# Kernel tuning notes

Hardware: AMD Instinct MI355X
Metric: run time of the kernel (lower is better)

The kernel has to match this reference:

```python
import jax, jax.numpy as jnp
import numpy as np

TEMP = 1.0
EULER_GAMMA = 0.5772156649015329
BIG = 1.0e9


def setup_inputs() -> dict:
    key = jax.random.key(0)
    k = jax.random.split(key, 8)
    B, N, D, H = 32, 1024, 1024, 512  # batch, seq, d_model, hidden_size//2
    queries = jax.random.normal(k[0], (B, N, D), jnp.float32)
    queries_mask = jnp.ones((B, N), dtype=bool)
    W1 = jax.random.normal(k[1], (D, H), jnp.float32) * 0.02
    b1 = jnp.zeros((H,), jnp.float32)
    W2 = jax.random.normal(k[2], (H, 1), jnp.float32) * 0.02
    b2 = jnp.zeros((1,), jnp.float32)
    uniform_noise = jax.random.uniform(k[3], (B, N, 1), jnp.float32, 0.0, 1e-5)
    gumbel_noise = jax.random.gumbel(k[4], (B, N, 1), jnp.float32)
    return {"queries": queries, "queries_mask": queries_mask, "W1": W1, "b1": b1,
            "W2": W2, "b2": b2, "uniform_noise": uniform_noise,
            "gumbel_noise": gumbel_noise, "action_refinement": 1}


def reference(queries, queries_mask, W1, b1, W2, b2, uniform_noise, gumbel_noise, action_refinement):
    B, N, D = queries.shape
    # block0: Dense(H, relu) -> Dense(1); then softplus clamp + log + tiny uniform noise
    h = jax.nn.relu(jnp.einsum('bnd,dh->bnh', queries, W1) + b1)
    acts = jnp.einsum('bnh,ho->bno', h, W2) + b2                      # [B,N,1]
    acts = jnp.log(jnp.maximum(jax.nn.softplus(acts), 1e-5)) + uniform_noise
    acts = jnp.repeat(acts, action_refinement, axis=0)                # [BR,N,1]
    vmask = jnp.repeat(queries_mask[:, None, :].astype(jnp.float32), action_refinement, axis=0)  # [BR,1,N]
    n_valid = jnp.sum(vmask, axis=-1)                                 # [BR,1]
    mask_n1 = jnp.transpose(vmask, (0, 2, 1))                         # [BR,N,1]
    sqz_mask = mask_n1[..., 0]                                        # [BR,N]
    masked_acts = jnp.where(mask_n1 > 0, acts, -1e6)                  # [BR,N,1]
    perturb = masked_acts + gumbel_noise                              # [BR,N,1]
    # deterministic NeuralSort
    s = (jnp.exp(perturb) * mask_n1)[..., 0]                          # [BR,N]
    A = jnp.abs(s[:, :, None] - s[:, None, :])                        # [BR,N,N]
    Bmat = jnp.sum(A, axis=-1, keepdims=True)                         # A @ (1 1^T): row sums broadcast
    scaling = (N + 1 - 2 * (jnp.arange(N) + 1)).astype(jnp.float32)   # [N]
    C = s[:, :, None] * scaling[None, None, :]                        # [BR,N,N]
    P_hat = jnp.transpose(C - Bmat, (0, 2, 1)) - (1.0 - vmask) * BIG  # [BR,N,N]
    # greedy argmax permutation extraction (find_permu), vectorized over batch
    BR = P_hat.shape[0]
    def step(flag, row):                                              # row: [BR,N]
        tmp = row - flag * BIG
        idx = jnp.argmax(tmp, axis=-1)
        flag = jnp.maximum(flag, jax.nn.one_hot(idx, N, dtype=flag.dtype))
        return flag, idx
    _, idxs = jax.lax.scan(step, jnp.zeros((BR, N), jnp.float32), jnp.transpose(P_hat, (1, 0, 2)))
    chosen = jnp.transpose(idxs).astype(jnp.int32)                    # [BR,N]
    chosen = jnp.concatenate([jnp.zeros((BR, 1), jnp.int32), chosen[:, :-1]], axis=-1)
    id_permu = jnp.arange(N, dtype=jnp.int32)[None, :]
    permu = jnp.where(sqz_mask > 0, chosen, id_permu)                 # [BR,N]
    sample_permu = jax.nn.one_hot(permu, N, axis=-1, dtype=jnp.float32)
    # Plackett-Luce log-likelihood of sampled permutation
    exp_actis = jnp.exp(jnp.take_along_axis(masked_acts[..., 0], permu, axis=-1))
    rev_cumsum = jnp.cumsum(exp_actis[:, ::-1], axis=-1)[:, ::-1]
    eps = 1e-20
    log_nom = (jnp.log(exp_actis + eps) - jnp.log(rev_cumsum + eps)) * sqz_mask
    log_nom = jnp.sum(log_nom, axis=-1, keepdims=True)                # [BR,1]
    log_norm = jnp.zeros_like(log_nom)
    # KL term
    sqz_acts = acts[..., 0]
    kl1 = n_valid * (np.log(TEMP) - 1.0 + EULER_GAMMA * (1.0 / TEMP - 1.0))
    s1 = (1.0 / TEMP) * jnp.sum(sqz_acts * sqz_mask, axis=-1).reshape(-1, 1)
    s2 = jnp.sum(jnp.exp(-1.0 / TEMP * jnp.maximum(sqz_acts * sqz_mask, -20.0 * TEMP)), axis=-1).reshape(-1, 1) - (jnp.float32(N) - n_valid)
    kl = kl1 + s1 + s2 * jnp.exp(jax.lax.lgamma(jnp.float32(1.0 + 1.0 / TEMP)))
    return sample_permu, masked_acts[..., 0], kl, log_nom, log_norm
```

## Files before the change

kernel.cpp:

```cpp
#include <hip/hip_runtime.h>
#include <math.h>

#define BB 32
#define NN 1024
#define DD 1024
#define HH 512

#define OUT0_OFF 0
#define OUT1_OFF (BB * NN * NN)
#define OUT2_OFF (OUT1_OFF + BB * NN)
#define OUT3_OFF (OUT2_OFF + BB)
#define OUT4_OFF (OUT3_OFF + BB)

#define WS_ACTS 0
#define WS_W1T  131072
#define WS_RANK 1179648

typedef __attribute__((ext_vector_type(8))) short short8;
typedef __attribute__((ext_vector_type(4))) float floatx4;

__device__ inline unsigned int f2bf(float x) {
    unsigned int u = __builtin_bit_cast(unsigned int, x);
    return (u + 0x7FFFu + ((u >> 16) & 1u)) >> 16;
}

__global__ __launch_bounds__(1024) void w1t_kernel(const float* __restrict__ W1,
                                                   unsigned short* __restrict__ W1T)
{
    __shared__ float T[32][33];
    const int tx = threadIdx.x, ty = threadIdx.y;
    const int d0 = blockIdx.x * 32, h0 = blockIdx.y * 32;
    T[ty][tx] = W1[(d0 + ty) * HH + h0 + tx];
    __syncthreads();
    W1T[(size_t)(h0 + ty) * DD + d0 + tx] = (unsigned short)f2bf(T[tx][ty]);
}

#define ASTRIDE 40
#define MT 128
__global__ __launch_bounds__(512, 2) void gemm_acts_kernel(
    const float* __restrict__ q, const unsigned short* __restrict__ W1T,
    const float* __restrict__ b1, const float* __restrict__ W2,
    const float* __restrict__ b2, const float* __restrict__ unoise,
    float* __restrict__ acts_ws, float* __restrict__ out1)
{
    __shared__ short As[MT * ASTRIDE];
    __shared__ short Bs[HH * ASTRIDE];
    __shared__ float red[MT][4];

    const int tid = threadIdx.x;
    const int w = tid >> 6;
    const int lane = tid & 63;
    const int c = lane & 15;
    const int qd = lane >> 4;
    const int wr = (w >> 2) * 64;
    const int wc = (w & 3) * 128;
    const int m0 = blockIdx.x * MT;

    floatx4 acc[8][4];
    #pragma unroll
    for (int tn = 0; tn < 8; ++tn)
        #pragma unroll
        for (int tm = 0; tm < 4; ++tm)
            acc[tn][tm] = (floatx4){0.f, 0.f, 0.f, 0.f};

    const int srow = tid >> 2;
    const int skp  = tid & 3;
    const float* aptr = q + (size_t)(m0 + srow) * DD + skp * 8;
    const uint4* w1t4 = (const uint4*)W1T;

    float4 a0, a1;
    uint4 bv[4];

    {
        const float4* ap = (const float4*)aptr;
        a0 = ap[0]; a1 = ap[1];
        #pragma unroll
        for (int ii = 0; ii < 4; ++ii)
            bv[ii] = w1t4[(size_t)(ii * 128 + srow) * 128 + skp];
    }

    #pragma unroll 1
    for (int kk = 0; kk < 32; ++kk) {
        {
            uint4 pk;
            pk.x = f2bf(a0.x) | (f2bf(a0.y) << 16);
            pk.y = f2bf(a0.z) | (f2bf(a0.w) << 16);
            pk.z = f2bf(a1.x) | (f2bf(a1.y) << 16);
            pk.w = f2bf(a1.z) | (f2bf(a1.w) << 16);
            *(uint4*)(&As[srow * ASTRIDE + skp * 8]) = pk;
            #pragma unroll
            for (int ii = 0; ii < 4; ++ii)
                *(uint4*)(&Bs[(ii * 128 + srow) * ASTRIDE + skp * 8]) = bv[ii];
        }
        __syncthreads();
        if (kk < 31) {
            const float4* ap = (const float4*)(aptr + (kk + 1) * 32);
            a0 = ap[0]; a1 = ap[1];
            #pragma unroll
            for (int ii = 0; ii < 4; ++ii)
                bv[ii] = w1t4[(size_t)(ii * 128 + srow) * 128 + (kk + 1) * 4 + skp];
        }
        short8 af[4];
        #pragma unroll
        for (int tm = 0; tm < 4; ++tm)
            af[tm] = *(const short8*)(&As[(wr + tm * 16 + c) * ASTRIDE + qd * 8]);
        #pragma unroll
        for (int tn = 0; tn < 8; ++tn) {
            short8 bf = *(const short8*)(&Bs[(wc + tn * 16 + c) * ASTRIDE + qd * 8]);
            #pragma unroll
            for (int tm = 0; tm < 4; ++tm)
                acc[tn][tm] = __builtin_amdgcn_mfma_f32_16x16x32_bf16(
                    af[tm], bf, acc[tn][tm], 0, 0, 0);
        }
        __syncthreads();
    }

    float b1v[8], w2v[8];
    #pragma unroll
    for (int tn = 0; tn < 8; ++tn) {
        int col = wc + tn * 16 + c;
        b1v[tn] = b1[col];
        w2v[tn] = W2[col];
    }
    #pragma unroll
    for (int tm = 0; tm < 4; ++tm) {
        #pragma unroll
        for (int r = 0; r < 4; ++r) {
            float p = 0.f;
            #pragma unroll
            for (int tn = 0; tn < 8; ++tn) {
                float v = acc[tn][tm][r] + b1v[tn];
                p = fmaf(fmaxf(v, 0.f), w2v[tn], p);
            }
            p += __shfl_xor(p, 1);
            p += __shfl_xor(p, 2);
            p += __shfl_xor(p, 4);
            p += __shfl_xor(p, 8);
            if (c == 0) red[wr + tm * 16 + qd * 4 + r][w & 3] = p;
        }
    }
    __syncthreads();
    if (tid < MT) {
        float raw = red[tid][0] + red[tid][1] + red[tid][2] + red[tid][3] + b2[0];
        float sp = fmaxf(raw, 0.f) + log1pf(expf(-fabsf(raw)));
        int row = m0 + tid;
        float av = logf(fmaxf(sp, 1e-5f)) + unoise[row];
        acts_ws[row] = av;
        out1[row]    = av;
    }
}

__global__ __launch_bounds__(256) void zero_kernel(float4* __restrict__ p, int n4)
{
    int idx = blockIdx.x * blockDim.x + threadIdx.x;
    int stride = gridDim.x * blockDim.x;
    float4 z = make_float4(0.f, 0.f, 0.f, 0.f);
    for (int i = idx; i < n4; i += stride) p[i] = z;
}

__global__ __launch_bounds__(256) void rank_kernel(
    const float* __restrict__ acts_ws, const float* __restrict__ gumbel,
    int* __restrict__ rank)
{
    __shared__ float P[NN];
    const int b = blockIdx.x >> 2;
    const int chunk = blockIdx.x & 3;
    const int tid = threadIdx.x;
    #pragma unroll
    for (int r = 0; r < 4; ++r) {
        int j = r * 256 + tid;
        P[j] = acts_ws[b * NN + j] + gumbel[b * NN + j];
    }
    __syncthreads();
    const int i = chunk * 256 + tid;
    const float pert = P[i];
    int cnt = 0;
    const float4* P4 = (const float4*)P;
    for (int j4 = 0; j4 < NN / 4; ++j4) {
        float4 pv = P4[j4];
        int j = j4 * 4;
        cnt += (pv.x > pert) || (pv.x == pert && j + 0 < i);
        cnt += (pv.y > pert) || (pv.y == pert && j + 1 < i);
        cnt += (pv.z > pert) || (pv.z == pert && j + 2 < i);
        cnt += (pv.w > pert) || (pv.w == pert && j + 3 < i);
    }
    rank[b * NN + i] = cnt;
}

__global__ __launch_bounds__(1024) void permu_stats_kernel(
    const float* __restrict__ acts_ws, const int* __restrict__ rank,
    float* __restrict__ out0, float* __restrict__ out2,
    float* __restrict__ out3, float* __restrict__ out4)
{
    __shared__ float A[NN];
    __shared__ int   IDX[NN];
    __shared__ float WT[16];
    __shared__ float WSUF[17];
    __shared__ float P0[16], P1[16], P2[16];

    const int b = blockIdx.x;
    const int i = threadIdx.x;
    const int lane = i & 63;
    const int w = i >> 6;

    float a = acts_ws[b * NN + i];
    A[i] = a;
    IDX[rank[b * NN + i]] = i;
    __syncthreads();

    int perm = (i == 0) ? 0 : IDX[i - 1];
    out0[((size_t)b * NN + i) * NN + perm] = 1.0f;

    float e = expf(A[perm]);
    float s = e;
    #pragma unroll
    for (int off = 1; off < 64; off <<= 1) {
        float v = __shfl_down(s, off);
        if (lane + off < 64) s += v;
    }
    if (lane == 0) WT[w] = s;
    __syncthreads();
    if (w == 0) {
        float t = (lane < 16) ? WT[lane] : 0.f;
        #pragma unroll
        for (int off = 1; off < 16; off <<= 1) {
            float v = __shfl_down(t, off);
            if (lane + off < 16) t += v;
        }
        if (lane < 16) WSUF[lane] = t;
        if (lane == 0) WSUF[16] = 0.f;
    }
    __syncthreads();

    float S = s + WSUF[w + 1];
    float term = logf(e + 1e-20f) - logf(S + 1e-20f);

    float r0 = term, r1 = a, r2 = expf(-fmaxf(a, -20.f));
    #pragma unroll
    for (int off = 1; off < 64; off <<= 1) {
        r0 += __shfl_xor(r0, off);
        r1 += __shfl_xor(r1, off);
        r2 += __shfl_xor(r2, off);
    }
    if (lane == 0) { P0[w] = r0; P1[w] = r1; P2[w] = r2; }
    __syncthreads();
    if (i == 0) {
        float t0 = 0.f, t1 = 0.f, t2 = 0.f;
        #pragma unroll
        for (int k = 0; k < 16; ++k) { t0 += P0[k]; t1 += P1[k]; t2 += P2[k]; }
        out3[b] = t0;
        out2[b] = -(float)NN + t1 + t2;
        out4[b] = 0.f;
    }
}

extern "C" void kernel_launch(void* const* d_in, const int* in_sizes, int n_in,
                              void* d_out, int out_size, void* d_ws, size_t ws_size,
                              hipStream_t stream)
{
    const float* q      = (const float*)d_in[0];
    const float* W1     = (const float*)d_in[2];
    const float* b1     = (const float*)d_in[3];
    const float* W2     = (const float*)d_in[4];
    const float* b2     = (const float*)d_in[5];
    const float* unoise = (const float*)d_in[6];
    const float* gumbel = (const float*)d_in[7];

    float* out  = (float*)d_out;
    char*  ws   = (char*)d_ws;
    float*          acts = (float*)(ws + WS_ACTS);
    unsigned short* W1T  = (unsigned short*)(ws + WS_W1T);
    int*            rank = (int*)(ws + WS_RANK);

    w1t_kernel<<<dim3(32, 16), dim3(32, 32), 0, stream>>>(W1, W1T);
    gemm_acts_kernel<<<(BB * NN) / MT, 512, 0, stream>>>(q, W1T, b1, W2, b2,
                                                         unoise, acts,
                                                         out + OUT1_OFF);
    zero_kernel<<<8192, 256, 0, stream>>>((float4*)(out + OUT0_OFF),
                                          (BB * NN * NN) / 4);
    rank_kernel<<<BB * 4, 256, 0, stream>>>(acts, gumbel, rank);
    permu_stats_kernel<<<BB, 1024, 0, stream>>>(acts, rank,
                                                out + OUT0_OFF, out + OUT2_OFF,
                                                out + OUT3_OFF, out + OUT4_OFF);
}
```

Baseline: 377.8 us.

## Double-buffer GEMM tiles with direct global-to-LDS loads and XOR swizzle

Restructures the fused MLP GEMM to use double-buffered LDS tiles, loading W1T tiles straight from global memory into LDS with global_load_lds and an XOR-swizzled layout instead of padded rows. The M-tile shrinks from 128 to 64 rows with 256 threads per block, so each block has 4 waves covering all 512 hidden columns. The aim is to overlap the next tile's loads with the MFMA work and remove register staging plus one barrier per k-step. The cost is twice as many blocks re-reading W1T and a manual waitcnt/barrier scheme that must be correct.

Result: faster. 315.7 us (-16.4%).

```diff
diff --git a/kernel.cpp b/kernel.cpp
--- a/kernel.cpp
+++ b/kernel.cpp
@@ -24,6 +24,12 @@
     return (u + 0x7FFFu + ((u >> 16) & 1u)) >> 16;
 }
 
+__device__ inline void gload_lds16(const void* g, void* l) {
+    __builtin_amdgcn_global_load_lds(
+        (const __attribute__((address_space(1))) unsigned int*)g,
+        (__attribute__((address_space(3))) unsigned int*)l, 16, 0, 0);
+}
+
 __global__ __launch_bounds__(1024) void w1t_kernel(const float* __restrict__ W1,
                                                    unsigned short* __restrict__ W1T)
 {
@@ -35,26 +41,23 @@
     W1T[(size_t)(h0 + ty) * DD + d0 + tx] = (unsigned short)f2bf(T[tx][ty]);
 }
 
-#define ASTRIDE 40
-#define MT 128
-__global__ __launch_bounds__(512, 2) void gemm_acts_kernel(
+#define MT 64
+__global__ __launch_bounds__(256, 2) void gemm_acts_kernel(
     const float* __restrict__ q, const unsigned short* __restrict__ W1T,
     const float* __restrict__ b1, const float* __restrict__ W2,
     const float* __restrict__ b2, const float* __restrict__ unoise,
     float* __restrict__ acts_ws, float* __restrict__ out1)
 {
-    __shared__ short As[MT * ASTRIDE];
-    __shared__ short Bs[HH * ASTRIDE];
+    __shared__ short As[2][MT * 32];
+    __shared__ short Bs[2][HH * 32];
     __shared__ float red[MT][4];
 
-    const int tid = threadIdx.x;
-    const int w = tid >> 6;
+    const int tid  = threadIdx.x;
+    const int w    = tid >> 6;
     const int lane = tid & 63;
-    const int c = lane & 15;
-    const int qd = lane >> 4;
-    const int wr = (w >> 2) * 64;
-    const int wc = (w & 3) * 128;
-    const int m0 = blockIdx.x * MT;
+    const int c    = lane & 15;
+    const int qd   = lane >> 4;
+    const int m0   = blockIdx.x * MT;
 
     floatx4 acc[8][4];
     #pragma unroll
@@ -63,62 +66,93 @@
         for (int tm = 0; tm < 4; ++tm)
             acc[tn][tm] = (floatx4){0.f, 0.f, 0.f, 0.f};
 
-    const int srow = tid >> 2;
-    const int skp  = tid & 3;
+    int boff[8];
+    #pragma unroll
+    for (int j = 0; j < 8; ++j) {
+        int n  = (w * 8 + j) * 16 + (lane >> 2);
+        int c0 = (lane & 3) * 16;
+        int s  = (n >> 1) & 3;
+        boff[j] = n * 2048 + (c0 ^ (s << 4));
+    }
+    const char* w1tb = (const char*)W1T;
+
+    const int srow = tid >> 2, skp = tid & 3;
     const float* aptr = q + (size_t)(m0 + srow) * DD + skp * 8;
-    const uint4* w1t4 = (const uint4*)W1T;
+    const int asw = (skp * 16) ^ (((srow >> 1) & 3) << 4);
+
+    int aoff[4], boffr[8];
+    #pragma unroll
+    for (int tm = 0; tm < 4; ++tm) {
+        int r = tm * 16 + c;
+        aoff[tm] = r * 64 + ((qd * 16) ^ (((r >> 1) & 3) << 4));
+    }
+    #pragma unroll
+    for (int tn = 0; tn < 8; ++tn) {
+        int n = w * 128 + tn * 16 + c;
+        boffr[tn] = n * 64 + ((qd * 16) ^ (((n >> 1) & 3) << 4));
+    }
 
     float4 a0, a1;
-    uint4 bv[4];
-
+
+    #pragma unroll
+    for (int j = 0; j < 8; ++j)
+        gload_lds16(w1tb + boff[j], (char*)(&Bs[0][0]) + (w * 8 + j) * 1024);
     {
         const float4* ap = (const float4*)aptr;
-        a0 = ap[0]; a1 = ap[1];
-        #pragma unroll
-        for (int ii = 0; ii < 4; ++ii)
-            bv[ii] = w1t4[(size_t)(ii * 128 + srow) * 128 + skp];
-    }
+        float4 v0 = ap[0], v1 = ap[1];
+        uint4 pk;
+        pk.x = f2bf(v0.x) | (f2bf(v0.y) << 16);
+        pk.y = f2bf(v0.z) | (f2bf(v0.w) << 16);
+        pk.z = f2bf(v1.x) | (f2bf(v1.y) << 16);
+        pk.w = f2bf(v1.z) | (f2bf(v1.w) << 16);
+        *(uint4*)((char*)(&As[0][0]) + srow * 64 + asw) = pk;
+        const float4* ap1 = (const float4*)(aptr + 32);
+        a0 = ap1[0]; a1 = ap1[1];
+    }
+    asm volatile("s_waitcnt vmcnt(0) lgkmcnt(0)" ::: "memory");
+    __builtin_amdgcn_s_barrier();
 
     #pragma unroll 1
     for (int kk = 0; kk < 32; ++kk) {
+        const int cur = kk & 1, nxt = cur ^ 1;
+        const int kb = (kk < 31) ? kk + 1 : 31;
+        #pragma unroll
+        for (int j = 0; j < 8; ++j)
+            gload_lds16(w1tb + (boff[j] + kb * 64),
+                        (char*)(&Bs[nxt][0]) + (w * 8 + j) * 1024);
         {
             uint4 pk;
             pk.x = f2bf(a0.x) | (f2bf(a0.y) << 16);
             pk.y = f2bf(a0.z) | (f2bf(a0.w) << 16);
             pk.z = f2bf(a1.x) | (f2bf(a1.y) << 16);
             pk.w = f2bf(a1.z) | (f2bf(a1.w) << 16);
-            *(uint4*)(&As[srow * ASTRIDE + skp * 8]) = pk;
-            #pragma unroll
-            for (int ii = 0; ii < 4; ++ii)
-                *(uint4*)(&Bs[(ii * 128 + srow) * ASTRIDE + skp * 8]) = bv[ii];
-        }
-        __syncthreads();
-        if (kk < 31) {
-            const float4* ap = (const float4*)(aptr + (kk + 1) * 32);
+            *(uint4*)((char*)(&As[nxt][0]) + srow * 64 + asw) = pk;
+        }
+        {
+            const int ka = (kk < 30) ? kk + 2 : 31;
+            const float4* ap = (const float4*)(aptr + ka * 32);
             a0 = ap[0]; a1 = ap[1];
-            #pragma unroll
-            for (int ii = 0; ii < 4; ++ii)
-                bv[ii] = w1t4[(size_t)(ii * 128 + srow) * 128 + (kk + 1) * 4 + skp];
         }
         short8 af[4];
         #pragma unroll
         for (int tm = 0; tm < 4; ++tm)
-            af[tm] = *(const short8*)(&As[(wr + tm * 16 + c) * ASTRIDE + qd * 8]);
+            af[tm] = *(const short8*)((const char*)(&As[cur][0]) + aoff[tm]);
         #pragma unroll
         for (int tn = 0; tn < 8; ++tn) {
-            short8 bf = *(const short8*)(&Bs[(wc + tn * 16 + c) * ASTRIDE + qd * 8]);
+            short8 bf = *(const short8*)((const char*)(&Bs[cur][0]) + boffr[tn]);
             #pragma unroll
             for (int tm = 0; tm < 4; ++tm)
                 acc[tn][tm] = __builtin_amdgcn_mfma_f32_16x16x32_bf16(
                     af[tm], bf, acc[tn][tm], 0, 0, 0);
         }
-        __syncthreads();
+        asm volatile("s_waitcnt vmcnt(0) lgkmcnt(0)" ::: "memory");
+        __builtin_amdgcn_s_barrier();
     }
 
     float b1v[8], w2v[8];
     #pragma unroll
     for (int tn = 0; tn < 8; ++tn) {
-        int col = wc + tn * 16 + c;
+        int col = w * 128 + tn * 16 + c;
         b1v[tn] = b1[col];
         w2v[tn] = W2[col];
     }
@@ -136,7 +170,7 @@
             p += __shfl_xor(p, 2);
             p += __shfl_xor(p, 4);
             p += __shfl_xor(p, 8);
-            if (c == 0) red[wr + tm * 16 + qd * 4 + r][w & 3] = p;
+            if (c == 0) red[tm * 16 + qd * 4 + r][w] = p;
         }
     }
     __syncthreads();
@@ -273,7 +307,7 @@
     int*            rank = (int*)(ws + WS_RANK);
 
     w1t_kernel<<<dim3(32, 16), dim3(32, 32), 0, stream>>>(W1, W1T);
-    gemm_acts_kernel<<<(BB * NN) / MT, 512, 0, stream>>>(q, W1T, b1, W2, b2,
+    gemm_acts_kernel<<<(BB * NN) / MT, 256, 0, stream>>>(q, W1T, b1, W2, b2,
                                                          unoise, acts,
                                                          out + OUT1_OFF);
     zero_kernel<<<8192, 256, 0, stream>>>((float4*)(out + OUT0_OFF),
```

## Pre-swizzle W1 into MFMA fragment layout and drop LDS staging in GEMM

Applied to the files above, without the earlier changes.

W1 is now converted once into bf16 fragments laid out exactly as each lane's MFMA B operand needs them. The GEMM kernel then loads A and B fragments straight from global memory into registers, with no shared-memory staging and no per-iteration barriers. The M tile shrinks to 64 rows with 256 threads, and bf16 conversion uses the hardware packed-convert instruction. This removes LDS traffic and synchronisation, but relies on L2/L1 for reuse of the B fragments and has no explicit prefetching, so memory latency may be exposed.

New measurement: 345.3 us. 1.09x faster.

```diff
diff --git a/kernel.cpp b/kernel.cpp
--- a/kernel.cpp
+++ b/kernel.cpp
@@ -18,43 +18,50 @@
 
 typedef __attribute__((ext_vector_type(8))) short short8;
 typedef __attribute__((ext_vector_type(4))) float floatx4;
-
-__device__ inline unsigned int f2bf(float x) {
-    unsigned int u = __builtin_bit_cast(unsigned int, x);
-    return (u + 0x7FFFu + ((u >> 16) & 1u)) >> 16;
-}
-
-__global__ __launch_bounds__(1024) void w1t_kernel(const float* __restrict__ W1,
-                                                   unsigned short* __restrict__ W1T)
-{
-    __shared__ float T[32][33];
-    const int tx = threadIdx.x, ty = threadIdx.y;
-    const int d0 = blockIdx.x * 32, h0 = blockIdx.y * 32;
-    T[ty][tx] = W1[(d0 + ty) * HH + h0 + tx];
-    __syncthreads();
-    W1T[(size_t)(h0 + ty) * DD + d0 + tx] = (unsigned short)f2bf(T[tx][ty]);
-}
-
-#define ASTRIDE 40
-#define MT 128
-__global__ __launch_bounds__(512, 2) void gemm_acts_kernel(
-    const float* __restrict__ q, const unsigned short* __restrict__ W1T,
+typedef __attribute__((ext_vector_type(4))) unsigned int uintx4;
+
+__device__ inline unsigned int cvtpk(float a, float b) {
+    unsigned int r;
+    asm("v_cvt_pk_bf16_f32 %0, %1, %2" : "=v"(r) : "v"(a), "v"(b));
+    return r;
+}
+
+__global__ __launch_bounds__(64) void w1t_kernel(const float* __restrict__ W1,
+                                                 unsigned short* __restrict__ Bfrag)
+{
+    const int s  = blockIdx.x;
+    const int tn = blockIdx.y;
+    const int l  = threadIdx.x;
+    const int c  = l & 15, qd = l >> 4;
+    const int n  = tn * 16 + c;
+    float v[8];
+    #pragma unroll
+    for (int e = 0; e < 8; ++e)
+        v[e] = W1[(size_t)(s * 32 + qd * 8 + e) * HH + n];
+    uintx4 u;
+    u.x = cvtpk(v[0], v[1]);
+    u.y = cvtpk(v[2], v[3]);
+    u.z = cvtpk(v[4], v[5]);
+    u.w = cvtpk(v[6], v[7]);
+    *(uintx4*)(Bfrag + ((size_t)(s * 32 + tn) * 64 + l) * 8) = u;
+}
+
+#define MT 64
+
+__global__ __launch_bounds__(256, 2) void gemm_acts_kernel(
+    const float* __restrict__ q, const unsigned short* __restrict__ Bfrag,
     const float* __restrict__ b1, const float* __restrict__ W2,
     const float* __restrict__ b2, const float* __restrict__ unoise,
     float* __restrict__ acts_ws, float* __restrict__ out1)
 {
-    __shared__ short As[MT * ASTRIDE];
-    __shared__ short Bs[HH * ASTRIDE];
     __shared__ float red[MT][4];
 
-    const int tid = threadIdx.x;
-    const int w = tid >> 6;
+    const int tid  = threadIdx.x;
+    const int w    = tid >> 6;
     const int lane = tid & 63;
-    const int c = lane & 15;
-    const int qd = lane >> 4;
-    const int wr = (w >> 2) * 64;
-    const int wc = (w & 3) * 128;
-    const int m0 = blockIdx.x * MT;
+    const int c    = lane & 15;
+    const int qd   = lane >> 4;
+    const int m0   = blockIdx.x * MT;
 
     floatx4 acc[8][4];
     #pragma unroll
@@ -63,62 +70,42 @@
         for (int tm = 0; tm < 4; ++tm)
             acc[tn][tm] = (floatx4){0.f, 0.f, 0.f, 0.f};
 
-    const int srow = tid >> 2;
-    const int skp  = tid & 3;
-    const float* aptr = q + (size_t)(m0 + srow) * DD + skp * 8;
-    const uint4* w1t4 = (const uint4*)W1T;
-
-    float4 a0, a1;
-    uint4 bv[4];
-
-    {
-        const float4* ap = (const float4*)aptr;
-        a0 = ap[0]; a1 = ap[1];
-        #pragma unroll
-        for (int ii = 0; ii < 4; ++ii)
-            bv[ii] = w1t4[(size_t)(ii * 128 + srow) * 128 + skp];
-    }
-
-    #pragma unroll 1
-    for (int kk = 0; kk < 32; ++kk) {
-        {
-            uint4 pk;
-            pk.x = f2bf(a0.x) | (f2bf(a0.y) << 16);
-            pk.y = f2bf(a0.z) | (f2bf(a0.w) << 16);
-            pk.z = f2bf(a1.x) | (f2bf(a1.y) << 16);
-            pk.w = f2bf(a1.z) | (f2bf(a1.w) << 16);
-            *(uint4*)(&As[srow * ASTRIDE + skp * 8]) = pk;
-            #pragma unroll
-            for (int ii = 0; ii < 4; ++ii)
-                *(uint4*)(&Bs[(ii * 128 + srow) * ASTRIDE + skp * 8]) = bv[ii];
-        }
-        __syncthreads();
-        if (kk < 31) {
-            const float4* ap = (const float4*)(aptr + (kk + 1) * 32);
-            a0 = ap[0]; a1 = ap[1];
-            #pragma unroll
-            for (int ii = 0; ii < 4; ++ii)
-                bv[ii] = w1t4[(size_t)(ii * 128 + srow) * 128 + (kk + 1) * 4 + skp];
-        }
+    const float* aptr[4];
+    #pragma unroll
+    for (int tm = 0; tm < 4; ++tm)
+        aptr[tm] = q + (size_t)(m0 + tm * 16 + c) * DD + qd * 8;
+
+    const short8* bp = (const short8*)Bfrag;
+    const int bbase = w * 8 * 64 + lane;
+
+    #pragma unroll 2
+    for (int s = 0; s < 32; ++s) {
         short8 af[4];
         #pragma unroll
-        for (int tm = 0; tm < 4; ++tm)
-            af[tm] = *(const short8*)(&As[(wr + tm * 16 + c) * ASTRIDE + qd * 8]);
+        for (int tm = 0; tm < 4; ++tm) {
+            float4 v0 = *(const float4*)(aptr[tm] + s * 32);
+            float4 v1 = *(const float4*)(aptr[tm] + s * 32 + 4);
+            uintx4 u;
+            u.x = cvtpk(v0.x, v0.y);
+            u.y = cvtpk(v0.z, v0.w);
+            u.z = cvtpk(v1.x, v1.y);
+            u.w = cvtpk(v1.z, v1.w);
+            af[tm] = __builtin_bit_cast(short8, u);
+        }
         #pragma unroll
         for (int tn = 0; tn < 8; ++tn) {
-            short8 bf = *(const short8*)(&Bs[(wc + tn * 16 + c) * ASTRIDE + qd * 8]);
+            short8 bf = bp[(size_t)s * 32 * 64 + bbase + tn * 64];
             #pragma unroll
             for (int tm = 0; tm < 4; ++tm)
                 acc[tn][tm] = __builtin_amdgcn_mfma_f32_16x16x32_bf16(
                     af[tm], bf, acc[tn][tm], 0, 0, 0);
         }
-        __syncthreads();
     }
 
     float b1v[8], w2v[8];
     #pragma unroll
     for (int tn = 0; tn < 8; ++tn) {
-        int col = wc + tn * 16 + c;
+        int col = w * 128 + tn * 16 + c;
         b1v[tn] = b1[col];
         w2v[tn] = W2[col];
     }
@@ -136,7 +123,7 @@
             p += __shfl_xor(p, 2);
             p += __shfl_xor(p, 4);
             p += __shfl_xor(p, 8);
-            if (c == 0) red[wr + tm * 16 + qd * 4 + r][w & 3] = p;
+            if (c == 0) red[tm * 16 + qd * 4 + r][w] = p;
         }
     }
     __syncthreads();
@@ -268,12 +255,12 @@
 
     float* out  = (float*)d_out;
     char*  ws   = (char*)d_ws;
-    float*          acts = (float*)(ws + WS_ACTS);
-    unsigned short* W1T  = (unsigned short*)(ws + WS_W1T);
-    int*            rank = (int*)(ws + WS_RANK);
-
-    w1t_kernel<<<dim3(32, 16), dim3(32, 32), 0, stream>>>(W1, W1T);
-    gemm_acts_kernel<<<(BB * NN) / MT, 512, 0, stream>>>(q, W1T, b1, W2, b2,
+    float*          acts  = (float*)(ws + WS_ACTS);
+    unsigned short* Bfrag = (unsigned short*)(ws + WS_W1T);
+    int*            rank  = (int*)(ws + WS_RANK);
+
+    w1t_kernel<<<dim3(32, 32), 64, 0, stream>>>(W1, Bfrag);
+    gemm_acts_kernel<<<(BB * NN) / MT, 256, 0, stream>>>(q, Bfrag, b1, W2, b2,
                                                          unoise, acts,
                                                          out + OUT1_OFF);
     zero_kernel<<<8192, 256, 0, stream>>>((float4*)(out + OUT0_OFF),
```
